# Performance work log

Hardware: AMD Instinct MI355X
Metric: run time of the kernel (lower is better)

Reference implementation:

```python
import jax, jax.numpy as jnp
import numpy as np

B, N, D, H = 32, 2048, 65, 64  # batch, seq_len, in_dim+out_dim, hid
GAMMA = 0.0001


def setup_inputs() -> dict:
    key = jax.random.key(0)
    kx, kq, kk, kv = jax.random.split(key, 4)
    x = jax.random.normal(kx, (B, N, D), dtype=jnp.float32)
    std_qk = (GAMMA / D) ** 0.5
    Wq = jax.random.normal(kq, (H, D), dtype=jnp.float32) * std_qk
    Wk = jax.random.normal(kk, (H, D), dtype=jnp.float32) * std_qk
    Wv = jax.random.normal(kv, (D, D), dtype=jnp.float32) * GAMMA
    return {"x": x, "Wq": Wq, "Wk": Wk, "Wv": Wv}


def reference(x, Wq, Wk, Wv):
    # Linear projections (torch nn.Linear: x @ W^T)
    Q = jnp.einsum('bnd,hd->bnh', x, Wq)  # [B, N, H]
    K = jnp.einsum('bnd,hd->bnh', x, Wk)  # [B, N, H]
    V = jnp.einsum('bnd,ed->bne', x, Wv)  # [B, N, D]
    # Non-softmax linear attention: (Q K^T) V, as written in the module
    scores = jnp.einsum('bnh,bmh->bnm', Q, K)  # [B, N, N]
    out = jnp.einsum('bnm,bmd->bnd', scores, V)  # [B, N, D]
    return out
```

## Files before the change

kernel.cpp:

```cpp
#include <hip/hip_runtime.h>

#define BB 32
#define NN 2048
#define DD 65
#define HH 64
#define ST 68
#define TILE (DD * ST)
#define CC 32

__device__ __forceinline__ float4 f4add(float4 a, float4 b) {
  return make_float4(a.x + b.x, a.y + b.y, a.z + b.z, a.w + b.w);
}

__global__ __launch_bounds__(256) void k1_gram(const float* __restrict__ x,
                                               float* __restrict__ P) {
  __shared__ __align__(16) float Xl[64 * ST];
  const int t = (int)threadIdx.x;
  const int tx = t & 15, ty = t >> 4;
  const int blk = (int)blockIdx.x;
  const int b = blk >> 5, c = blk & 31;
  const float* src = x + ((size_t)b * NN + (size_t)c * 64) * DD;

  {
    float tmp[17];
#pragma unroll
    for (int q = 0; q < 17; q++) {
      const int idx = t + 256 * q;
      if (idx < 64 * DD) tmp[q] = src[idx];
    }
#pragma unroll
    for (int q = 0; q < 17; q++) {
      const int idx = t + 256 * q;
      if (idx < 64 * DD) {
        const int r = idx / DD;
        Xl[r * ST + (idx - r * DD)] = tmp[q];
      }
    }
  }
  __syncthreads();

  float g[4][4] = {};
  float g64[4] = {};
  float gcc = 0.f;
  for (int n = 0; n < 64; n++) {
    float rowf[4], colf[4];
    *(float4*)rowf = *(const float4*)&Xl[n * ST + 4 * ty];
    *(float4*)colf = *(const float4*)&Xl[n * ST + 4 * tx];
#pragma unroll
    for (int r = 0; r < 4; r++)
#pragma unroll
      for (int cc = 0; cc < 4; cc++)
        g[r][cc] = fmaf(rowf[r], colf[cc], g[r][cc]);
    if (ty == 0) {
      float x64 = Xl[n * ST + 64];
#pragma unroll
      for (int cc = 0; cc < 4; cc++) g64[cc] = fmaf(x64, colf[cc], g64[cc]);
      if (tx == 0) gcc = fmaf(x64, x64, gcc);
    }
  }
  float* Pp = P + (size_t)blk * TILE;
#pragma unroll
  for (int r = 0; r < 4; r++)
    *(float4*)&Pp[(4 * ty + r) * ST + 4 * tx] = *(float4*)g[r];
  if (ty == 0) {
    *(float4*)&Pp[64 * ST + 4 * tx] = *(float4*)g64;
#pragma unroll
    for (int cc = 0; cc < 4; cc++)
      Pp[(4 * tx + cc) * ST + 64] = g64[cc];
    if (tx == 0) Pp[64 * ST + 64] = gcc;
  }
}

__global__ __launch_bounds__(256) void kred(const float* __restrict__ P,
                                            float* __restrict__ G) {
  const int t = (int)threadIdx.x;
  const int blk = (int)blockIdx.x;
  const int b = blk / 5, s = blk - b * 5;
  const int Q = TILE / 4;
  const int i4 = s * 256 + t;
  if (i4 < Q) {
    const float4* Pb = (const float4*)(P + (size_t)b * CC * TILE);
    float4 acc = make_float4(0.f, 0.f, 0.f, 0.f);
#pragma unroll
    for (int grp = 0; grp < 4; grp++) {
      float4 v[8];
#pragma unroll
      for (int cc = 0; cc < 8; cc++)
        v[cc] = Pb[(size_t)(8 * grp + cc) * Q + i4];
#pragma unroll
      for (int stp = 4; stp >= 1; stp >>= 1)
#pragma unroll
        for (int cc = 0; cc < stp; cc++) v[cc] = f4add(v[cc], v[cc + stp]);
      acc = f4add(acc, v[0]);
    }
    ((float4*)(G + (size_t)b * TILE))[i4] = acc;
  }
}

__global__ __launch_bounds__(256) void k2_chain(
    const float* __restrict__ Wq, const float* __restrict__ Wk,
    const float* __restrict__ Wv, const float* __restrict__ G,
    float* __restrict__ Tm) {
  __shared__ __align__(16) float WqL[HH * ST];
  __shared__ __align__(16) float WkL[HH * ST];
  __shared__ __align__(16) float GL[TILE];
  __shared__ __align__(16) float WvT[TILE];
  __shared__ __align__(16) float Mr[8 * ST];
  __shared__ __align__(16) float Rr[8 * ST];

  const int t = (int)threadIdx.x;
  const int tx = t & 31, ty = t >> 5;
  const int blk = (int)blockIdx.x;
  const int b = blk / 9, rg = blk - b * 9;
  const int i = 8 * rg + ty;
  const bool alive = (i < DD);
  const int ic = alive ? i : 0;

  {
    float tq[17], tk[17];
#pragma unroll
    for (int q = 0; q < 17; q++) {
      const int idx = t + 256 * q;
      if (idx < HH * DD) { tq[q] = Wq[idx]; tk[q] = Wk[idx]; }
    }
#pragma unroll
    for (int q = 0; q < 17; q++) {
      const int idx = t + 256 * q;
      if (idx < HH * DD) {
        const int r = idx / DD, cc = idx - r * DD;
        WqL[r * ST + cc] = tq[q];
        WkL[r * ST + cc] = tk[q];
      }
    }
  }
  {
    const float4* Gb4 = (const float4*)(G + (size_t)b * TILE);
    float4 tG[5];
#pragma unroll
    for (int q = 0; q < 5; q++) {
      const int i4 = t + 256 * q;
      if (i4 < TILE / 4) tG[q] = Gb4[i4];
    }
#pragma unroll
    for (int q = 0; q < 5; q++) {
      const int i4 = t + 256 * q;
      if (i4 < TILE / 4) *((float4*)GL + i4) = tG[q];
    }
  }
  {
    float tv[17];
#pragma unroll
    for (int q = 0; q < 17; q++) {
      const int idx = t + 256 * q;
      if (idx < DD * DD) tv[q] = Wv[idx];
    }
#pragma unroll
    for (int q = 0; q < 17; q++) {
      const int idx = t + 256 * q;
      if (idx < DD * DD) {
        const int j = idx / DD, k = idx - j * DD;
        WvT[k * ST + j] = tv[q];
      }
    }
  }
  __syncthreads();

  {
    float m0 = 0.f, m1 = 0.f, m2 = 0.f;
    for (int h = 0; h < HH; h++) {
      const float wq = WqL[h * ST + ic];
      m0 = fmaf(wq, WkL[h * ST + tx], m0);
      m1 = fmaf(wq, WkL[h * ST + tx + 32], m1);
      m2 = fmaf(wq, WkL[h * ST + 64], m2);
    }
    if (alive) {
      Mr[ty * ST + tx] = m0;
      Mr[ty * ST + tx + 32] = m1;
      if (tx == 0) Mr[ty * ST + 64] = m2;
    }
  }
  __syncthreads();

  {
    float r0 = 0.f, r1 = 0.f, r2 = 0.f;
    for (int k = 0; k < DD; k++) {
      const float mm = Mr[ty * ST + k];
      r0 = fmaf(mm, GL[k * ST + tx], r0);
      r1 = fmaf(mm, GL[k * ST + tx + 32], r1);
      r2 = fmaf(mm, GL[k * ST + 64], r2);
    }
    if (alive) {
      Rr[ty * ST + tx] = r0;
      Rr[ty * ST + tx + 32] = r1;
      if (tx == 0) Rr[ty * ST + 64] = r2;
    }
  }
  __syncthreads();

  {
    float t0 = 0.f, t1 = 0.f, t2 = 0.f;
    for (int k = 0; k < DD; k++) {
      const float rv = Rr[ty * ST + k];
      t0 = fmaf(rv, WvT[k * ST + tx], t0);
      t1 = fmaf(rv, WvT[k * ST + tx + 32], t1);
      t2 = fmaf(rv, WvT[k * ST + 64], t2);
    }
    if (alive) {
      float* Tb = Tm + (size_t)b * TILE + (size_t)i * ST;
      Tb[tx] = t0;
      Tb[tx + 32] = t1;
      if (tx == 0) Tb[64] = t2;
    }
  }
}

__global__ __launch_bounds__(256) void k3_out(const float* __restrict__ x,
                                              const float* __restrict__ Tt,
                                              float* __restrict__ out) {
  __shared__ __align__(16) float Tl[TILE];
  __shared__ __align__(16) float Xl[64 * ST];
  const int t = (int)threadIdx.x;
  const int tx = t & 15, ty = t >> 4;
  const int blk = (int)blockIdx.x;
  const int b = blk >> 5;
  const int rb = (blk & 31) * 64;
  const float4* Tg4 = (const float4*)(Tt + (size_t)b * TILE);
  const float* src = x + ((size_t)b * NN + rb) * DD;
  {
    float4 tT[5];
    float tX[17];
#pragma unroll
    for (int q = 0; q < 5; q++) {
      const int i4 = t + 256 * q;
      if (i4 < TILE / 4) tT[q] = Tg4[i4];
    }
#pragma unroll
    for (int q = 0; q < 17; q++) {
      const int idx = t + 256 * q;
      if (idx < 64 * DD) tX[q] = src[idx];
    }
#pragma unroll
    for (int q = 0; q < 5; q++) {
      const int i4 = t + 256 * q;
      if (i4 < TILE / 4) *((float4*)Tl + i4) = tT[q];
    }
#pragma unroll
    for (int q = 0; q < 17; q++) {
      const int idx = t + 256 * q;
      if (idx < 64 * DD) {
        const int r = idx / DD;
        Xl[r * ST + (idx - r * DD)] = tX[q];
      }
    }
  }
  __syncthreads();

  float o[4][4] = {}, o64[4] = {};
  for (int kk = 0; kk < 64; kk += 4) {
    float xa4[4][4];
#pragma unroll
    for (int r = 0; r < 4; r++)
      *(float4*)xa4[r] = *(const float4*)&Xl[(4 * ty + r) * ST + kk];
#pragma unroll
    for (int e = 0; e < 4; e++) {
      const int k = kk + e;
      float tb[4];
      *(float4*)tb = *(const float4*)&Tl[k * ST + 4 * tx];
#pragma unroll
      for (int r = 0; r < 4; r++)
#pragma unroll
        for (int cc = 0; cc < 4; cc++)
          o[r][cc] = fmaf(xa4[r][e], tb[cc], o[r][cc]);
      if (tx == 0) {
        float t64 = Tl[k * ST + 64];
#pragma unroll
        for (int r = 0; r < 4; r++) o64[r] = fmaf(xa4[r][e], t64, o64[r]);
      }
    }
  }
  {
    float xs[4];
#pragma unroll
    for (int r = 0; r < 4; r++) xs[r] = Xl[(4 * ty + r) * ST + 64];
    float tb[4];
    *(float4*)tb = *(const float4*)&Tl[64 * ST + 4 * tx];
#pragma unroll
    for (int r = 0; r < 4; r++)
#pragma unroll
      for (int cc = 0; cc < 4; cc++)
        o[r][cc] = fmaf(xs[r], tb[cc], o[r][cc]);
    if (tx == 0) {
      float t64 = Tl[64 * ST + 64];
#pragma unroll
      for (int r = 0; r < 4; r++) o64[r] = fmaf(xs[r], t64, o64[r]);
    }
  }

  float* ob = out + ((size_t)b * NN + rb) * DD;
#pragma unroll
  for (int r = 0; r < 4; r++)
#pragma unroll
    for (int cc = 0; cc < 4; cc++)
      ob[(4 * ty + r) * DD + 4 * tx + cc] = o[r][cc];
  if (tx == 0) {
#pragma unroll
    for (int r = 0; r < 4; r++) ob[(4 * ty + r) * DD + 64] = o64[r];
  }
}

extern "C" void kernel_launch(void* const* d_in, const int* in_sizes, int n_in,
                              void* d_out, int out_size, void* d_ws,
                              size_t ws_size, hipStream_t stream) {
  const float* x = (const float*)d_in[0];
  const float* Wq = (const float*)d_in[1];
  const float* Wk = (const float*)d_in[2];
  const float* Wv = (const float*)d_in[3];
  float* out = (float*)d_out;

  float* P = (float*)d_ws;
  float* G = P + (size_t)BB * CC * TILE;
  float* Tm = G + (size_t)BB * TILE;

  k1_gram<<<BB * CC, 256, 0, stream>>>(x, P);
  kred<<<BB * 5, 256, 0, stream>>>(P, G);
  k2_chain<<<BB * 9, 256, 0, stream>>>(Wq, Wk, Wv, G, Tm);
  k3_out<<<BB * CC, 256, 0, stream>>>(x, Tm, out);
  (void)in_sizes; (void)n_in; (void)out_size; (void)ws_size;
}
```

Measured before the change: 145.7 us.

## Use direct global-to-LDS loads, staged output stores, and occupancy hints in gram/out kernels

k3_out now loads the T tile with global_load_lds straight into shared memory and splits the x staging into two smaller register batches. Its output is written to LDS first and then stored with coalesced float4 writes instead of strided scalar stores. Both k1_gram and k3_out gain min-blocks launch bounds, and the divergent tx==0/ty==0 branches for column 64 are replaced with redundant uniform work. The goal is lower register pressure and higher occupancy plus better store coalescing, at the cost of extra LDS round-trips and some wasted FMAs.

```diff
diff --git a/kernel.cpp b/kernel.cpp
--- a/kernel.cpp
+++ b/kernel.cpp
@@ -12,8 +12,13 @@
   return make_float4(a.x + b.x, a.y + b.y, a.z + b.z, a.w + b.w);
 }
 
-__global__ __launch_bounds__(256) void k1_gram(const float* __restrict__ x,
-                                               float* __restrict__ P) {
+#define GL2LDS(g, l)                                             \
+  __builtin_amdgcn_global_load_lds(                              \
+      (const __attribute__((address_space(1))) void*)(g),        \
+      (__attribute__((address_space(3))) void*)(l), 16, 0, 0)
+
+__global__ __launch_bounds__(256, 6) void k1_gram(const float* __restrict__ x,
+                                                  float* __restrict__ P) {
   __shared__ __align__(16) float Xl[64 * ST];
   const int t = (int)threadIdx.x;
   const int tx = t & 15, ty = t >> 4;
@@ -22,18 +27,22 @@
   const float* src = x + ((size_t)b * NN + (size_t)c * 64) * DD;
 
   {
-    float tmp[17];
-#pragma unroll
-    for (int q = 0; q < 17; q++) {
-      const int idx = t + 256 * q;
-      if (idx < 64 * DD) tmp[q] = src[idx];
-    }
-#pragma unroll
-    for (int q = 0; q < 17; q++) {
-      const int idx = t + 256 * q;
-      if (idx < 64 * DD) {
-        const int r = idx / DD;
-        Xl[r * ST + (idx - r * DD)] = tmp[q];
+#pragma unroll
+    for (int p = 0; p < 3; p++) {
+      float tmp[6];
+      const int cnt = (p == 2) ? 5 : 6;
+#pragma unroll
+      for (int q = 0; q < 6; q++) {
+        const int idx = t + 256 * (6 * p + q);
+        if (q < cnt && idx < 64 * DD) tmp[q] = src[idx];
+      }
+#pragma unroll
+      for (int q = 0; q < 6; q++) {
+        const int idx = t + 256 * (6 * p + q);
+        if (q < cnt && idx < 64 * DD) {
+          const int r = idx / DD;
+          Xl[r * ST + (idx - r * DD)] = tmp[q];
+        }
       }
     }
   }
@@ -46,17 +55,15 @@
     float rowf[4], colf[4];
     *(float4*)rowf = *(const float4*)&Xl[n * ST + 4 * ty];
     *(float4*)colf = *(const float4*)&Xl[n * ST + 4 * tx];
+    const float x64 = Xl[n * ST + 64];
 #pragma unroll
     for (int r = 0; r < 4; r++)
 #pragma unroll
       for (int cc = 0; cc < 4; cc++)
         g[r][cc] = fmaf(rowf[r], colf[cc], g[r][cc]);
-    if (ty == 0) {
-      float x64 = Xl[n * ST + 64];
-#pragma unroll
-      for (int cc = 0; cc < 4; cc++) g64[cc] = fmaf(x64, colf[cc], g64[cc]);
-      if (tx == 0) gcc = fmaf(x64, x64, gcc);
-    }
+#pragma unroll
+    for (int cc = 0; cc < 4; cc++) g64[cc] = fmaf(x64, colf[cc], g64[cc]);
+    gcc = fmaf(x64, x64, gcc);
   }
   float* Pp = P + (size_t)blk * TILE;
 #pragma unroll
@@ -214,42 +221,45 @@
   }
 }
 
-__global__ __launch_bounds__(256) void k3_out(const float* __restrict__ x,
-                                              const float* __restrict__ Tt,
-                                              float* __restrict__ out) {
+__global__ __launch_bounds__(256, 4) void k3_out(const float* __restrict__ x,
+                                                 const float* __restrict__ Tt,
+                                                 float* __restrict__ out) {
   __shared__ __align__(16) float Tl[TILE];
   __shared__ __align__(16) float Xl[64 * ST];
   const int t = (int)threadIdx.x;
   const int tx = t & 15, ty = t >> 4;
+  const int wid = t >> 6, lane = t & 63;
   const int blk = (int)blockIdx.x;
   const int b = blk >> 5;
   const int rb = (blk & 31) * 64;
   const float4* Tg4 = (const float4*)(Tt + (size_t)b * TILE);
   const float* src = x + ((size_t)b * NN + rb) * DD;
-  {
-    float4 tT[5];
-    float tX[17];
-#pragma unroll
-    for (int q = 0; q < 5; q++) {
-      const int i4 = t + 256 * q;
-      if (i4 < TILE / 4) tT[q] = Tg4[i4];
-    }
-#pragma unroll
-    for (int q = 0; q < 17; q++) {
-      const int idx = t + 256 * q;
-      if (idx < 64 * DD) tX[q] = src[idx];
-    }
-#pragma unroll
-    for (int q = 0; q < 5; q++) {
-      const int i4 = t + 256 * q;
-      if (i4 < TILE / 4) *((float4*)Tl + i4) = tT[q];
-    }
-#pragma unroll
-    for (int q = 0; q < 17; q++) {
-      const int idx = t + 256 * q;
-      if (idx < 64 * DD) {
+
+#pragma unroll
+  for (int q = 0; q < 4; q++) {
+    const int s = q * 256 + wid * 64 + lane;
+    GL2LDS(Tg4 + s, Tl + (size_t)(q * 256 + wid * 64) * 4);
+  }
+  {
+    const int s = 1024 + wid * 64 + lane;
+    if (s < TILE / 4) GL2LDS(Tg4 + s, Tl + (size_t)(1024 + wid * 64) * 4);
+  }
+
+#pragma unroll
+  for (int p = 0; p < 2; p++) {
+    float tmp[9];
+    const int cnt = (p == 1) ? 8 : 9;
+#pragma unroll
+    for (int q = 0; q < 9; q++) {
+      const int idx = t + 256 * (9 * p + q);
+      if (q < cnt && idx < 64 * DD) tmp[q] = src[idx];
+    }
+#pragma unroll
+    for (int q = 0; q < 9; q++) {
+      const int idx = t + 256 * (9 * p + q);
+      if (q < cnt && idx < 64 * DD) {
         const int r = idx / DD;
-        Xl[r * ST + (idx - r * DD)] = tX[q];
+        Xl[r * ST + (idx - r * DD)] = tmp[q];
       }
     }
   }
@@ -258,24 +268,26 @@
   float o[4][4] = {}, o64[4] = {};
   for (int kk = 0; kk < 64; kk += 4) {
     float xa4[4][4];
+    float tb4[4][4];
+    float t64e[4];
 #pragma unroll
     for (int r = 0; r < 4; r++)
       *(float4*)xa4[r] = *(const float4*)&Xl[(4 * ty + r) * ST + kk];
 #pragma unroll
+    for (int e = 0; e < 4; e++)
+      *(float4*)tb4[e] = *(const float4*)&Tl[(kk + e) * ST + 4 * tx];
+#pragma unroll
+    for (int e = 0; e < 4; e++) t64e[e] = Tl[(kk + e) * ST + 64];
+#pragma unroll
     for (int e = 0; e < 4; e++) {
-      const int k = kk + e;
-      float tb[4];
-      *(float4*)tb = *(const float4*)&Tl[k * ST + 4 * tx];
 #pragma unroll
       for (int r = 0; r < 4; r++)
 #pragma unroll
         for (int cc = 0; cc < 4; cc++)
-          o[r][cc] = fmaf(xa4[r][e], tb[cc], o[r][cc]);
-      if (tx == 0) {
-        float t64 = Tl[k * ST + 64];
-#pragma unroll
-        for (int r = 0; r < 4; r++) o64[r] = fmaf(xa4[r][e], t64, o64[r]);
-      }
+          o[r][cc] = fmaf(xa4[r][e], tb4[e][cc], o[r][cc]);
+#pragma unroll
+      for (int r = 0; r < 4; r++)
+        o64[r] = fmaf(xa4[r][e], t64e[e], o64[r]);
     }
   }
   {
@@ -284,27 +296,37 @@
     for (int r = 0; r < 4; r++) xs[r] = Xl[(4 * ty + r) * ST + 64];
     float tb[4];
     *(float4*)tb = *(const float4*)&Tl[64 * ST + 4 * tx];
-#pragma unroll
-    for (int r = 0; r < 4; r++)
+    const float t64 = Tl[64 * ST + 64];
+#pragma unroll
+    for (int r = 0; r < 4; r++) {
 #pragma unroll
       for (int cc = 0; cc < 4; cc++)
         o[r][cc] = fmaf(xs[r], tb[cc], o[r][cc]);
-    if (tx == 0) {
-      float t64 = Tl[64 * ST + 64];
-#pragma unroll
-      for (int r = 0; r < 4; r++) o64[r] = fmaf(xs[r], t64, o64[r]);
-    }
-  }
-
-  float* ob = out + ((size_t)b * NN + rb) * DD;
-#pragma unroll
-  for (int r = 0; r < 4; r++)
+      o64[r] = fmaf(xs[r], t64, o64[r]);
+    }
+  }
+
+  __syncthreads();
+  float* Ol = Xl;
+#pragma unroll
+  for (int r = 0; r < 4; r++) {
 #pragma unroll
     for (int cc = 0; cc < 4; cc++)
-      ob[(4 * ty + r) * DD + 4 * tx + cc] = o[r][cc];
+      Ol[(4 * ty + r) * DD + 4 * tx + cc] = o[r][cc];
+  }
   if (tx == 0) {
 #pragma unroll
-    for (int r = 0; r < 4; r++) ob[(4 * ty + r) * DD + 64] = o64[r];
+    for (int r = 0; r < 4; r++) Ol[(4 * ty + r) * DD + 64] = o64[r];
+  }
+  __syncthreads();
+  {
+    float4* ob4 = (float4*)(out + ((size_t)b * NN + rb) * DD);
+    const float4* Ol4 = (const float4*)Ol;
+#pragma unroll
+    for (int q = 0; q < 5; q++) {
+      const int i4 = t + 256 * q;
+      if (i4 < (64 * DD) / 4) ob4[i4] = Ol4[i4];
+    }
   }
 }
 
```

Measured after the change: 117.1 us. -19.6%, faster.
